# Optimization experiments

Measured on AMD Instinct MI355X. Metric: run time of the kernel, lower is better.

Reference implementation:

```python
import jax, jax.numpy as jnp
import numpy as np

GAMMA = 0.99
STEP_TYPE_LAST = 2  # alf.data_structures.StepType.LAST
T, B = 256, 65536


def setup_inputs() -> dict:
    key = jax.random.key(0)
    k = jax.random.split(key, 7)
    return {
        "reward": jax.random.normal(k[0], (T, B), dtype=jnp.float32),
        "discount": jax.random.uniform(k[1], (T, B), dtype=jnp.float32),
        "value": jax.random.normal(k[2], (T, B), dtype=jnp.float32),
        "target_value": jax.random.normal(k[3], (T, B), dtype=jnp.float32),
        "step_type": jax.random.randint(k[4], (T, B), 0, 3, dtype=jnp.int32),
        "rollout_b": jax.random.randint(k[5], (T, B), 0, 2, dtype=jnp.int32),
        "train_b": jax.random.randint(k[6], (T, B), 0, 2, dtype=jnp.int32),
    }


def _discounted_return(rewards, values, is_lasts, discounts):
    # Backward recursion:
    #   rets[T-1] = values[T-1]; acc[T-1] = values[T-1]
    #   rets[t] = acc[t+1] * discounts[t+1] + rewards[t+1]
    #   acc[t]  = is_lasts[t] * values[t] + (1 - is_lasts[t]) * rets[t]
    # returns rets[0:T-1]  (shape [T-1, B])
    il = is_lasts.astype(values.dtype)
    xs = (discounts[1:], rewards[1:], il[:-1], values[:-1])
    xs_rev = jax.tree_util.tree_map(lambda x: x[::-1], xs)  # scan t = T-2 .. 0

    def step(acc, x):
        d, r, l, v = x
        ret = acc * d + r
        acc_new = l * v + (1.0 - l) * ret
        return acc_new, ret

    _, rets_rev = jax.lax.scan(step, values[-1], xs_rev)
    return jax.lax.stop_gradient(rets_rev[::-1])  # [T-1, B]


def reference(reward, discount, value, target_value, step_type, rollout_b, train_b):
    discounts = discount * GAMMA
    b = (rollout_b != 0) | (train_b != 0)
    b = b.at[0].set(False)
    is_lasts = (step_type == STEP_TYPE_LAST) | b
    returns = _discounted_return(reward, target_value, is_lasts, discounts)
    v = value[:-1]
    loss = jnp.square(returns - v)                 # element_wise_squared_loss
    loss = jnp.concatenate([loss, jnp.zeros_like(loss[:1])], axis=0)  # extend zero -> [T, B]
    return loss
```

## Files before the change

kernel.cpp:

```cpp
#include <hip/hip_runtime.h>
#include <hip/hip_bf16.h>

#define T_STEPS 256
#define B_COLS  65536
#define GAMMA_F 0.99f

__global__ __launch_bounds__(256) void td_loss_kernel(
    const float* __restrict__ reward,
    const float* __restrict__ discount,
    const float* __restrict__ value,
    const float* __restrict__ target_value,
    const int*   __restrict__ step_type,
    const int*   __restrict__ rollout_b,
    const int*   __restrict__ train_b,
    float*       __restrict__ out)
{
    const unsigned b = blockIdx.x * blockDim.x + threadIdx.x;

    const unsigned last = (unsigned)(T_STEPS - 1) * B_COLS + b;
    float acc = target_value[last];
    out[last] = 0.0f;

    #pragma unroll 4
    for (int i = T_STEPS - 2; i >= 1; --i) {
        const unsigned idx  = (unsigned)i * B_COLS + b;
        const unsigned idx1 = idx + B_COLS;

        const float d  = discount[idx1] * GAMMA_F;
        const float r  = reward[idx1];
        const float tv = target_value[idx];
        const float v  = value[idx];
        const int   st = step_type[idx];
        const int   rb = rollout_b[idx];
        const int   tb = train_b[idx];

        const float ret = fmaf(acc, d, r);
        const bool  l   = (st == 2) | (rb != 0) | (tb != 0);
        acc = l ? tv : ret;

        const float diff = ret - v;
        out[idx] = diff * diff;
    }

    {
        const unsigned idx  = b;
        const unsigned idx1 = B_COLS + b;
        const float d   = discount[idx1] * GAMMA_F;
        const float r   = reward[idx1];
        const float ret = fmaf(acc, d, r);
        const float v   = value[idx];
        const float diff = ret - v;
        out[idx] = diff * diff;
    }
}

extern "C" void kernel_launch(void* const* d_in, const int* in_sizes, int n_in,
                              void* d_out, int out_size, void* d_ws, size_t ws_size,
                              hipStream_t stream) {
    const float* reward       = (const float*)d_in[0];
    const float* discount     = (const float*)d_in[1];
    const float* value        = (const float*)d_in[2];
    const float* target_value = (const float*)d_in[3];
    const int*   step_type    = (const int*)d_in[4];
    const int*   rollout_b    = (const int*)d_in[5];
    const int*   train_b      = (const int*)d_in[6];
    float*       out          = (float*)d_out;

    const int block = 256;
    const int grid  = B_COLS / block;
    td_loss_kernel<<<grid, block, 0, stream>>>(
        reward, discount, value, target_value, step_type, rollout_b, train_b, out);
}
```

Before: 408.7 us.

## Parallelize backward recursion over time chunks with affine-composition scan

Splits the T dimension into 8 chunks of 32 steps, each handled by a separate group of 32 threads. Each group composes its chunk's recurrence as an affine map (P, Q), and a short serial scan in shared memory resolves the boundary values. This is meant to expose far more parallelism and memory-level concurrency than one serial thread per column. In exchange it keeps 96 floats per thread in registers and needs two block barriers, and each wavefront now covers only 32 contiguous columns, so loads are narrower.

```diff
diff --git a/kernel.cpp b/kernel.cpp
--- a/kernel.cpp
+++ b/kernel.cpp
@@ -4,8 +4,12 @@
 #define T_STEPS 256
 #define B_COLS  65536
 #define GAMMA_F 0.99f
+#define CHUNK   32
+#define NCHUNK  8
+#define COLS_PB 32
 
-__global__ __launch_bounds__(256) void td_loss_kernel(
+
+__global__ __launch_bounds__(256, 4) void td_loss_kernel(
     const float* __restrict__ reward,
     const float* __restrict__ discount,
     const float* __restrict__ value,
@@ -15,42 +19,67 @@
     const int*   __restrict__ train_b,
     float*       __restrict__ out)
 {
-    const unsigned b = blockIdx.x * blockDim.x + threadIdx.x;
+    const int col   = threadIdx.x & (COLS_PB - 1);
+    const int chunk = threadIdx.x >> 5;
+    const unsigned colg = blockIdx.x * COLS_PB + col;
 
-    const unsigned last = (unsigned)(T_STEPS - 1) * B_COLS + b;
-    float acc = target_value[last];
-    out[last] = 0.0f;
+    const int  hi  = chunk * CHUNK + (CHUNK - 1);
+    const bool top = (hi == T_STEPS - 1);
 
-    #pragma unroll 4
-    for (int i = T_STEPS - 2; i >= 1; --i) {
-        const unsigned idx  = (unsigned)i * B_COLS + b;
-        const unsigned idx1 = idx + B_COLS;
+    float p[CHUNK], q[CHUNK], vv[CHUNK];
+    float P = 1.0f, Q = 0.0f;
 
-        const float d  = discount[idx1] * GAMMA_F;
-        const float r  = reward[idx1];
+    #pragma unroll
+    for (int j = 0; j < CHUNK; ++j) {
+        const int i  = hi - j;
+        const int i1 = (j == 0 && top) ? i : (i + 1);
+        const unsigned idx  = (unsigned)i  * B_COLS + colg;
+        const unsigned idx1 = (unsigned)i1 * B_COLS + colg;
+
+        const float dp = discount[idx1] * GAMMA_F;
+        const float rp = reward[idx1];
         const float tv = target_value[idx];
-        const float v  = value[idx];
-        const int   st = step_type[idx];
-        const int   rb = rollout_b[idx];
-        const int   tb = train_b[idx];
+        vv[j] = value[idx];
+        const int st = step_type[idx];
+        const int rb = rollout_b[idx];
+        const int tb = train_b[idx];
 
-        const float ret = fmaf(acc, d, r);
-        const bool  l   = (st == 2) | (rb != 0) | (tb != 0);
-        acc = l ? tv : ret;
+        bool l = (st == 2) | (rb != 0) | (tb != 0);
+        if (j == 0) l = l | top;
 
-        const float diff = ret - v;
-        out[idx] = diff * diff;
+        p[j] = P * dp;
+        q[j] = fmaf(Q, dp, rp);
+        P = l ? 0.0f : p[j];
+        Q = l ? tv   : q[j];
     }
 
-    {
-        const unsigned idx  = b;
-        const unsigned idx1 = B_COLS + b;
-        const float d   = discount[idx1] * GAMMA_F;
-        const float r   = reward[idx1];
-        const float ret = fmaf(acc, d, r);
-        const float v   = value[idx];
-        const float diff = ret - v;
-        out[idx] = diff * diff;
+    __shared__ float sA [NCHUNK][COLS_PB];
+    __shared__ float sB [NCHUNK][COLS_PB];
+    __shared__ float sAl[NCHUNK][COLS_PB];
+    sA[chunk][col] = P;
+    sB[chunk][col] = Q;
+    __syncthreads();
+    if (threadIdx.x < COLS_PB) {
+        const int c = threadIdx.x;
+        float alpha = 0.0f;
+        #pragma unroll
+        for (int k = NCHUNK - 1; k >= 0; --k) {
+            sAl[k][c] = alpha;
+            alpha = fmaf(sA[k][c], alpha, sB[k][c]);
+        }
+    }
+    __syncthreads();
+    const float alpha = sAl[chunk][col];
+
+    #pragma unroll
+    for (int j = 0; j < CHUNK; ++j) {
+        const int i = hi - j;
+        const unsigned idx = (unsigned)i * B_COLS + colg;
+        const float ret  = fmaf(p[j], alpha, q[j]);
+        const float diff = ret - vv[j];
+        float o = diff * diff;
+        if (j == 0 && top) o = 0.0f;
+        out[idx] = o;
     }
 }
 
@@ -66,8 +95,8 @@
     const int*   train_b      = (const int*)d_in[6];
     float*       out          = (float*)d_out;
 
-    const int block = 256;
-    const int grid  = B_COLS / block;
+    const int block = NCHUNK * COLS_PB;
+    const int grid  = B_COLS / COLS_PB;
     td_loss_kernel<<<grid, block, 0, stream>>>(
         reward, discount, value, target_value, step_type, rollout_b, train_b, out);
 }
```

Result: slower. 472.5 us (+15.6%).
